# Kernel tuning notes

Hardware: AMD Instinct MI355X
Metric: run time of the kernel (lower is better)

The kernel has to match this reference:

```python
import jax, jax.numpy as jnp
import numpy as np

B, L, H, NH, DH, V, NL = 256, 100, 384, 12, 32, 30000, 6
FF = 4 * H


def _gelu(x):
    c = np.sqrt(2.0 / np.pi).astype(np.float32)
    return x * (0.5 * (1.0 + jnp.tanh(c * (x + 0.044715 * x ** 3))))


def _norm(X, g, b):
    mu = jnp.mean(X, axis=2, keepdims=True)
    var = jnp.var(X, axis=2, ddof=1, keepdims=True)  # torch.var is unbiased
    return g * ((X - mu) / jnp.sqrt(var + 1e-8)) + b


def setup_inputs():
    key = jax.random.key(0)
    ks = jax.random.split(key, 24)
    s = 0.02
    return {
        'x': jax.random.randint(ks[0], (B, L), 0, V, dtype=jnp.int32),
        'seg': jax.random.randint(ks[1], (B, L), 0, 3, dtype=jnp.int32),
        'tok_emb': jax.random.uniform(ks[2], (V, H), jnp.float32, -s, s),
        'seg_emb': jax.random.uniform(ks[3], (3, H), jnp.float32, -s, s),
        'pos_emb': jax.random.normal(ks[4], (L, H), jnp.float32) * 0.05,
        'Wq': jax.random.normal(ks[5], (NL, H, H), jnp.float32) * np.sqrt(2.0 / H).astype(np.float32),
        'bq': jnp.zeros((NL, H), jnp.float32),
        'Wk': jax.random.normal(ks[6], (NL, H, H), jnp.float32) * np.sqrt(2.0 / H).astype(np.float32),
        'bk': jnp.zeros((NL, H), jnp.float32),
        'Wv': jax.random.normal(ks[7], (NL, H, H), jnp.float32) * np.sqrt(2.0 / H).astype(np.float32),
        'bv': jnp.zeros((NL, H), jnp.float32),
        'Wo': jax.random.normal(ks[8], (NL, H, H), jnp.float32) * np.sqrt(2.0 / (2 * H)).astype(np.float32),
        'bo': jnp.zeros((NL, H), jnp.float32),
        'g1': jnp.ones((NL,), jnp.float32),
        'be1': jnp.zeros((NL,), jnp.float32),
        'W1': jax.random.normal(ks[9], (NL, H, FF), jnp.float32) * np.sqrt(2.0 / (H + FF)).astype(np.float32),
        'b1': jnp.zeros((NL, FF), jnp.float32),
        'W2': jax.random.normal(ks[10], (NL, FF, H), jnp.float32) * np.sqrt(2.0 / (H + FF)).astype(np.float32),
        'b2': jnp.zeros((NL, H), jnp.float32),
        'g2': jnp.ones((NL,), jnp.float32),
        'be2': jnp.zeros((NL,), jnp.float32),
        'dropout': 0,
    }


def _encoder_layer(h, pad_mask, nonpad, Wq, bq, Wk, bk, Wv, bv, Wo, bo, g1, be1, W1, b1, W2, b2, g2, be2):
    # --- multi-head self-attention (interleaved head split, as in source) ---
    q = (h @ Wq + bq).reshape(B, L, DH, NH).transpose(3, 0, 1, 2)  # (NH,B,L,DH)
    k = (h @ Wk + bk).reshape(B, L, DH, NH).transpose(3, 0, 3 - 1, 1)  # placeholder
    k = (h @ Wk + bk).reshape(B, L, DH, NH).transpose(3, 0, 2, 1)      # (NH,B,DH,L)
    v = (h @ Wv + bv).reshape(B, L, DH, NH).transpose(3, 0, 1, 2)      # (NH,B,L,DH)
    scale = 1.0 / np.sqrt(H).astype(np.float32)  # d_k = de.shape[-1] = hidden_dim!
    e = jnp.einsum('hbld,hbdm->hblm', q, k) * scale                    # (NH,B,L,L)
    e = jnp.where(pad_mask[None], -1e10, e)
    alpha = jax.nn.softmax(e, axis=-1)
    heads = jnp.einsum('hblm,hbmd->hbld', alpha, v)                    # (NH,B,L,DH)
    a = heads.transpose(1, 2, 0, 3).reshape(B, L, H)  # cat over heads on feature dim
    attn = _norm(a @ Wo + bo + h, g1, be1)
    attn = attn * nonpad
    # --- FFN ---
    f = _gelu(attn @ W1 + b1)
    f = f @ W2 + b2
    out = _norm(f + attn, g2, be2)
    return out * nonpad


def reference(x, seg, tok_emb, seg_emb, pos_emb, Wq, bq, Wk, bk, Wv, bv, Wo, bo,
              g1, be1, W1, b1, W2, b2, g2, be2, dropout):
    pad_mask = (x == 0)[:, None, :] * jnp.ones((1, L, 1), bool)  # (B,L,L)
    nonpad = (x != 0).astype(jnp.float32)[:, :, None]            # (B,L,1), bcast over H
    h = tok_emb[x] + seg_emb[seg] + pos_emb[None, :L]
    h = h * nonpad
    acc = h  # cumulative-sum skip connections: input_i = x_i + ... + x_1
    out = h
    for i in range(NL):
        out = _encoder_layer(acc, pad_mask, nonpad,
                             Wq[i], bq[i], Wk[i], bk[i], Wv[i], bv[i], Wo[i], bo[i],
                             g1[i], be1[i], W1[i], b1[i], W2[i], b2[i], g2[i], be2[i])
        acc = acc + out
    return out
```

## Files before the change

kernel.cpp:

```cpp
#include <hip/hip_runtime.h>
#include <hip/hip_bf16.h>
#include <math.h>

#define B_  256
#define L_  100
#define H_  384
#define NH_ 12
#define DH_ 32
#define NL_ 6
#define FF_ 1536
#define M_  (B_*L_)
#define QKVN 1152

#define LW     3538944
#define OFF_Q  0
#define OFF_K  294912
#define OFF_V  589824
#define OFF_WO 884736
#define OFF_W1 1179648
#define OFF_W2 2359296

typedef __attribute__((ext_vector_type(8))) short short8;
typedef __attribute__((ext_vector_type(4))) float f32x4;

#define GLOBAL_AS __attribute__((address_space(1)))
#define LDS_AS    __attribute__((address_space(3)))

__device__ __forceinline__ void gload_lds16(const void* g, void* l) {
    __builtin_amdgcn_global_load_lds((const GLOBAL_AS void*)g, (LDS_AS void*)l, 16, 0, 0);
}

__device__ __forceinline__ void split2(float v, __hip_bfloat16& hi, __hip_bfloat16& lo) {
    hi = __float2bfloat16(v);
    lo = __float2bfloat16(v - __bfloat162float(hi));
}

__device__ __forceinline__ unsigned short f2b(float v) {
    __hip_bfloat16 h = __float2bfloat16(v);
    return *(unsigned short*)&h;
}

#define VMW(N) asm volatile("s_waitcnt vmcnt(" #N ")" ::: "memory")

__global__ void embed_kernel(const int* __restrict__ x, const int* __restrict__ seg,
                             const float* __restrict__ tok, const float* __restrict__ sege,
                             const float* __restrict__ pos,
                             __hip_bfloat16* __restrict__ acc2) {
    int idx = blockIdx.x * blockDim.x + threadIdx.x;
    if (idx >= M_ * H_) return;
    int m = idx / H_;
    int f = idx - m * H_;
    int t = x[m];
    int s = seg[m];
    int l = m % L_;
    float v = tok[t * H_ + f] + sege[s * H_ + f] + pos[l * H_ + f];
    v = (t != 0) ? v : 0.0f;
    __hip_bfloat16 h, lo;
    split2(v, h, lo);
    acc2[(size_t)m * (2 * H_) + f]      = h;
    acc2[(size_t)m * (2 * H_) + H_ + f] = lo;
}

__global__ void transpose_all_kernel(const float* __restrict__ Wq, const float* __restrict__ Wk,
        const float* __restrict__ Wv, const float* __restrict__ Wo,
        const float* __restrict__ W1, const float* __restrict__ W2,
        __hip_bfloat16* __restrict__ wT) {
    __shared__ float tile[32][33];
    int l = blockIdx.x / 1728;
    int bid = blockIdx.x % 1728;
    const float* src;
    __hip_bfloat16* dst;
    int K, N, nx, tix, perm = 0;
    if (bid < 432) {
        int m = bid / 144; tix = bid % 144;
        src = (m == 0) ? Wq : (m == 1 ? Wk : Wv);
        src += (size_t)l * H_ * H_;
        dst = wT + (size_t)l * LW + (m == 0 ? OFF_Q : (m == 1 ? OFF_K : OFF_V));
        K = 384; N = 384; nx = 12; perm = 1;
    } else if (bid < 576) {
        tix = bid - 432; src = Wo + (size_t)l * H_ * H_;
        dst = wT + (size_t)l * LW + OFF_WO; K = 384; N = 384; nx = 12;
    } else if (bid < 1152) {
        tix = bid - 576; src = W1 + (size_t)l * H_ * FF_;
        dst = wT + (size_t)l * LW + OFF_W1; K = 384; N = 1536; nx = 48;
    } else {
        tix = bid - 1152; src = W2 + (size_t)l * FF_ * H_;
        dst = wT + (size_t)l * LW + OFF_W2; K = 1536; N = 384; nx = 12;
    }
    int n0 = (tix % nx) * 32, k0 = (tix / nx) * 32;
    int tx = threadIdx.x, ty = threadIdx.y;
    #pragma unroll
    for (int i = ty; i < 32; i += 8)
        tile[i][tx] = src[(size_t)(k0 + i) * N + (n0 + tx)];
    __syncthreads();
    #pragma unroll
    for (int i = ty; i < 32; i += 8) {
        float v = tile[tx][i];
        __hip_bfloat16 h, lo;
        split2(v, h, lo);
        int j = n0 + i;
        int jo = perm ? ((j % 12) * 32 + j / 12) : j;
        dst[(size_t)jo * (2 * K) + (k0 + tx)]     = h;
        dst[(size_t)jo * (2 * K) + K + (k0 + tx)] = lo;
    }
}

__global__ void bias_concat_kernel(const float* __restrict__ bq, const float* __restrict__ bk,
                                   const float* __restrict__ bv, float* __restrict__ out) {
    int i = blockIdx.x * 256 + threadIdx.x;
    if (i >= NL_ * QKVN) return;
    int l = i / QKVN, jp = i - l * QKVN;
    int t = jp / 384, r = jp % 384;
    int h = r >> 5, d = r & 31;
    int j = d * 12 + h;
    float v = (t == 0) ? bq[l * 384 + j] : (t == 1 ? bk[l * 384 + j] : bv[l * 384 + j]);
    out[i] = v;
}

template <int TAG, int BIG, int OMODE, int MODEK, int ACT>
__global__ __launch_bounds__(BIG ? 512 : 256) void gemm_bf16_kernel(
        const __hip_bfloat16* __restrict__ A2,
        const __hip_bfloat16* __restrict__ Wt2,
        const float* __restrict__ bias,
        void* __restrict__ outp,
        int N, int K, int nbx) {
    constexpr int BM = BIG ? 256 : 128;
    __shared__ __hip_bfloat16 As[3][BM * 32];
    __shared__ __hip_bfloat16 Bs[3][128 * 32];
    int t = threadIdx.x;
    int lane = t & 63, wv = t >> 6;
    int wm = wv >> 1, wn = wv & 1;

    int nwg = gridDim.x;
    int q8 = nwg >> 3, r8 = nwg & 7;
    int xcd = blockIdx.x & 7, off = blockIdx.x >> 3;
    int swz = (xcd < r8 ? xcd * (q8 + 1) : r8 * (q8 + 1) + (xcd - r8) * q8) + off;
    int bn = (swz % nbx) * 128;
    int bm = (swz / nbx) * BM;

    const int KstA = (MODEK == 2) ? K : 2 * K;
    const int KstW = 2 * K;
    const int Kend = (MODEK == 0) ? 3 * K : 2 * K;
    f32x4 acc[4][4] = {};

    int sr   = t >> 2;
    int sswz = (t & 3) ^ ((t >> 2) & 3) ^ ((t >> 4) & 3);
    const __hip_bfloat16* a_src = A2 + (size_t)(bm + sr) * KstA + sswz * 8;
    const __hip_bfloat16* b_src = Wt2 + (size_t)(bn + sr) * KstW + sswz * 8;

    int slotp = (lane >> 4) ^ (lane & 3) ^ ((lane >> 2) & 3);
    int aOff = (wm * 64 + (lane & 15)) * 32 + slotp * 8;
    int bOff = (wn * 64 + (lane & 15)) * 32 + slotp * 8;

#define STAGE(buf, ak, wk) do { \
        gload_lds16(a_src + (ak), &As[buf][wv * 512]); \
        gload_lds16(a_src + (size_t)(BM / 2) * KstA + (ak), &As[buf][(BM / 2) * 32 + wv * 512]); \
        gload_lds16(b_src + (wk), &Bs[buf][wv * 512]); \
        if (!BIG) gload_lds16(b_src + (size_t)64 * KstW + (wk), &Bs[buf][2048 + wv * 512]); \
    } while (0)

#define KOFFS(k0, ak, wk) do { \
        if (MODEK == 0) { ak = ((k0) < K) ? (k0) : (k0) - K; wk = ((k0) < 2 * K) ? (k0) : (k0) - 2 * K; } \
        else            { ak = ((k0) < K) ? (k0) : (k0) - K; wk = (k0); } \
    } while (0)

    int nt = Kend >> 5;
    {
        int ak, wk;
        KOFFS(0, ak, wk);
        STAGE(0, ak, wk);
        KOFFS(32, ak, wk);
        STAGE(1, ak, wk);
    }
    int c0 = 0, c1 = 1, c2 = 2;
    for (int ti = 0; ti < nt; ++ti) {
        if (ti + 2 < nt) {
            int k2 = (ti + 2) << 5;
            int ak, wk;
            KOFFS(k2, ak, wk);
            STAGE(c2, ak, wk);
            if (BIG) { VMW(6); } else { VMW(8); }
        } else if (ti + 2 == nt) {
            if (BIG) { VMW(3); } else { VMW(4); }
        } else {
            VMW(0);
        }
        __builtin_amdgcn_s_barrier();
        short8 af[4], bf[4];
        #pragma unroll
        for (int m = 0; m < 4; ++m) af[m] = *(const short8*)(&As[c0][aOff + m * 512]);
        #pragma unroll
        for (int n = 0; n < 4; ++n) bf[n] = *(const short8*)(&Bs[c0][bOff + n * 512]);
        __builtin_amdgcn_s_setprio(1);
        #pragma unroll
        for (int m = 0; m < 4; ++m)
            #pragma unroll
            for (int n = 0; n < 4; ++n)
                acc[m][n] = __builtin_amdgcn_mfma_f32_16x16x32_bf16(af[m], bf[n], acc[m][n], 0, 0, 0);
        __builtin_amdgcn_s_setprio(0);
        __builtin_amdgcn_s_barrier();
        int tmp = c0; c0 = c1; c1 = c2; c2 = tmp;
    }
#undef STAGE
#undef KOFFS

    int colBase = bn + wn * 64 + (lane & 15);
    int rowBase = bm + wm * 64 + (lane >> 4) * 4;
    const float c0f = 0.7978845608f;
    #pragma unroll
    for (int n = 0; n < 4; ++n) {
        int c = colBase + n * 16;
        float bvv = bias[c];
        #pragma unroll
        for (int m = 0; m < 4; ++m) {
            int r0 = rowBase + m * 16;
            #pragma unroll
            for (int r = 0; r < 4; ++r) {
                float v = acc[m][n][r] + bvv;
                if (ACT == 1) {
                    float u = c0f * (v + 0.044715f * v * v * v);
                    v = v / (1.0f + __expf(-2.0f * u));
                }
                size_t row = (size_t)(r0 + r);
                if (OMODE == 0) {
                    ((float*)outp)[row * N + c] = v;
                } else {
                    ((__hip_bfloat16*)outp)[row * N + c] = __float2bfloat16(v);
                }
            }
        }
    }
}

__global__ __launch_bounds__(256) void attn_kernel(const __hip_bfloat16* __restrict__ qkvP,
        const int* __restrict__ x, __hip_bfloat16* __restrict__ a2) {
    __shared__ unsigned short qs[112][32];
    __shared__ unsigned short ks[128][32];
    __shared__ unsigned short vst[32][136];
    __shared__ unsigned short ps[112][136];
    __shared__ int xb[128];
    int t = threadIdx.x;
    int lane = t & 63, wv = t >> 6;
    int b = blockIdx.x / NH_;
    int nh = blockIdx.x % NH_;
    const __hip_bfloat16* base = qkvP + (size_t)b * L_ * QKVN;

    for (int i = t; i < 576; i += 256) {
        int d = i / 18, w = i % 18;
        ((int*)vst)[d * 68 + 50 + w] = 0;
    }
    for (int i = t; i < 128; i += 256) xb[i] = (i < L_) ? x[b * L_ + i] : 0;

    {
        int r16 = lane >> 2, s = lane & 3;
        for (int i = wv; i < 7; i += 4) {
            int row = i * 16 + r16;
            int sp = s ^ (row & 3) ^ ((row >> 2) & 3);
            gload_lds16(base + (size_t)row * QKVN + nh * 32 + sp * 8, &qs[i * 16][0]);
        }
        for (int i = wv; i < 8; i += 4) {
            int row = i * 16 + r16;
            int sp = s ^ (row & 3) ^ ((row >> 2) & 3);
            gload_lds16(base + (size_t)row * QKVN + 384 + nh * 32 + sp * 8, &ks[i * 16][0]);
        }
    }
    if (t < 200) {
        int kv = t >> 1, d0 = (t & 1) * 16;
        const __hip_bfloat16* vsrc = base + (size_t)kv * QKVN + 768 + nh * 32 + d0;
        short8 v0 = *(const short8*)vsrc;
        short8 v1 = *(const short8*)(vsrc + 8);
        #pragma unroll
        for (int j = 0; j < 8; ++j) {
            vst[d0 + j][kv]     = (unsigned short)v0[j];
            vst[d0 + 8 + j][kv] = (unsigned short)v1[j];
        }
    }
    __syncthreads();

    const float scale = 1.0f / sqrtf((float)H_);
    int n = lane & 15, g = lane >> 4;

    for (int rt = wv; rt < 7; rt += 4) {
        int arow = rt * 16 + n;
        int asp = (g ^ (arow & 3) ^ ((arow >> 2) & 3)) * 8;
        short8 aq = *(const short8*)&qs[arow][asp];
        f32x4 s8[8];
        #pragma unroll
        for (int ct = 0; ct < 8; ++ct) {
            int brow = ct * 16 + n;
            int bsp = (g ^ (brow & 3) ^ ((brow >> 2) & 3)) * 8;
            short8 bk = *(const short8*)&ks[brow][bsp];
            f32x4 z = {0.0f, 0.0f, 0.0f, 0.0f};
            s8[ct] = __builtin_amdgcn_mfma_f32_16x16x32_bf16(aq, bk, z, 0, 0, 0);
        }
        #pragma unroll
        for (int ct = 0; ct < 8; ++ct) {
            int col = ct * 16 + n;
            int xv = xb[col];
            #pragma unroll
            for (int r = 0; r < 4; ++r) {
                float v = s8[ct][r] * scale;
                v = (xv == 0) ? -1e10f : v;
                v = (col >= L_) ? -INFINITY : v;
                s8[ct][r] = v;
            }
        }
        float sm[4];
        #pragma unroll
        for (int r = 0; r < 4; ++r) {
            float m = s8[0][r];
            #pragma unroll
            for (int ct = 1; ct < 8; ++ct) m = fmaxf(m, s8[ct][r]);
            m = fmaxf(m, __shfl_xor(m, 1, 16));
            m = fmaxf(m, __shfl_xor(m, 2, 16));
            m = fmaxf(m, __shfl_xor(m, 4, 16));
            m = fmaxf(m, __shfl_xor(m, 8, 16));
            float s = 0.0f;
            #pragma unroll
            for (int ct = 0; ct < 8; ++ct) {
                float p = __expf(s8[ct][r] - m);
                s8[ct][r] = p;
                s += p;
            }
            s += __shfl_xor(s, 1, 16);
            s += __shfl_xor(s, 2, 16);
            s += __shfl_xor(s, 4, 16);
            s += __shfl_xor(s, 8, 16);
            sm[r] = s;
        }
        int prow = rt * 16 + g * 4;
        #pragma unroll
        for (int ct = 0; ct < 8; ++ct) {
            int col = ct * 16 + n;
            #pragma unroll
            for (int r = 0; r < 4; ++r)
                ps[prow + r][col] = f2b(s8[ct][r]);
        }
        f32x4 o0 = {0.0f, 0.0f, 0.0f, 0.0f}, o1 = o0;
        #pragma unroll
        for (int kt = 0; kt < 4; ++kt) {
            short8 pa = *(const short8*)&ps[rt * 16 + n][kt * 32 + g * 8];
            short8 b0 = *(const short8*)&vst[n][kt * 32 + g * 8];
            short8 b1 = *(const short8*)&vst[16 + n][kt * 32 + g * 8];
            o0 = __builtin_amdgcn_mfma_f32_16x16x32_bf16(pa, b0, o0, 0, 0, 0);
            o1 = __builtin_amdgcn_mfma_f32_16x16x32_bf16(pa, b1, o1, 0, 0, 0);
        }
        #pragma unroll
        for (int r = 0; r < 4; ++r) {
            int lrow = prow + r;
            if (lrow < L_) {
                size_t row = (size_t)b * L_ + lrow;
                float inv = 1.0f / sm[r];
                __hip_bfloat16 h, lo;
                float v0 = o0[r] * inv;
                split2(v0, h, lo);
                a2[row * (2 * H_) + nh * DH_ + n]      = h;
                a2[row * (2 * H_) + H_ + nh * DH_ + n] = lo;
                float v1 = o1[r] * inv;
                split2(v1, h, lo);
                a2[row * (2 * H_) + nh * DH_ + 16 + n]      = h;
                a2[row * (2 * H_) + H_ + nh * DH_ + 16 + n] = lo;
            }
        }
    }
}

template <int MODE>
__global__ __launch_bounds__(128) void ln_kernel(
        const float* __restrict__ Xf,
        const __hip_bfloat16* __restrict__ R2,
        const int* __restrict__ x,
        const float* __restrict__ gp, const float* __restrict__ bp, int layer,
        float* __restrict__ Yf,
        __hip_bfloat16* __restrict__ Y2,
        __hip_bfloat16* __restrict__ acc2) {
    int row = blockIdx.x;
    int tid = threadIdx.x;
    size_t b1 = (size_t)row * H_;
    size_t b2 = (size_t)row * (2 * H_);

    float v[3];
    #pragma unroll
    for (int j = 0; j < 3; ++j) {
        int f = tid + j * 128;
        float r = __bfloat162float(R2[b2 + f]) + __bfloat162float(R2[b2 + H_ + f]);
        v[j] = Xf[b1 + f] + r;
    }

    __shared__ float red[2];
    float s = v[0] + v[1] + v[2];
    #pragma unroll
    for (int off = 32; off > 0; off >>= 1) s += __shfl_down(s, off);
    if ((tid & 63) == 0) red[tid >> 6] = s;
    __syncthreads();
    float mu = (red[0] + red[1]) * (1.0f / 384.0f);
    __syncthreads();

    float d[3];
    float qq = 0.0f;
    #pragma unroll
    for (int j = 0; j < 3; ++j) { d[j] = v[j] - mu; qq += d[j] * d[j]; }
    #pragma unroll
    for (int off = 32; off > 0; off >>= 1) qq += __shfl_down(qq, off);
    if ((tid & 63) == 0) red[tid >> 6] = qq;
    __syncthreads();
    float var = (red[0] + red[1]) * (1.0f / 383.0f);
    float rstd = rsqrtf(var + 1e-8f);

    float g = gp[layer], bb = bp[layer];
    float np_ = (x[row] != 0) ? 1.0f : 0.0f;
    #pragma unroll
    for (int j = 0; j < 3; ++j) {
        int f = tid + j * 128;
        float y = (g * (d[j] * rstd) + bb) * np_;
        if (MODE == 0) {
            __hip_bfloat16 h, lo;
            split2(y, h, lo);
            Y2[b2 + f]      = h;
            Y2[b2 + H_ + f] = lo;
        } else {
            Yf[b1 + f] = y;
            float a = __bfloat162float(acc2[b2 + f]) + __bfloat162float(acc2[b2 + H_ + f]) + y;
            __hip_bfloat16 h, lo;
            split2(a, h, lo);
            acc2[b2 + f]      = h;
            acc2[b2 + H_ + f] = lo;
        }
    }
}

extern "C" void kernel_launch(void* const* d_in, const int* in_sizes, int n_in,
                              void* d_out, int out_size, void* d_ws, size_t ws_size,
                              hipStream_t stream) {
    const int*   x    = (const int*)d_in[0];
    const int*   seg  = (const int*)d_in[1];
    const float* tok  = (const float*)d_in[2];
    const float* sege = (const float*)d_in[3];
    const float* pos  = (const float*)d_in[4];
    const float* Wq   = (const float*)d_in[5];
    const float* bq   = (const float*)d_in[6];
    const float* Wk   = (const float*)d_in[7];
    const float* bk   = (const float*)d_in[8];
    const float* Wv   = (const float*)d_in[9];
    const float* bv   = (const float*)d_in[10];
    const float* Wo   = (const float*)d_in[11];
    const float* bo   = (const float*)d_in[12];
    const float* g1   = (const float*)d_in[13];
    const float* be1  = (const float*)d_in[14];
    const float* W1   = (const float*)d_in[15];
    const float* b1   = (const float*)d_in[16];
    const float* W2   = (const float*)d_in[17];
    const float* b2   = (const float*)d_in[18];
    const float* g2   = (const float*)d_in[19];
    const float* be2  = (const float*)d_in[20];

    char* p = (char*)d_ws;
    __hip_bfloat16* wT   = (__hip_bfloat16*)p; p += (size_t)NL_ * LW * 2;
    __hip_bfloat16* acc2 = (__hip_bfloat16*)p; p += 39321600;
    __hip_bfloat16* bE2  = (__hip_bfloat16*)p; p += 39321600;
    float* qkvb          = (float*)p;          p += 27648;
    char* pool           = p;
    __hip_bfloat16* qkvP = (__hip_bfloat16*)pool;
    __hip_bfloat16* bA2  = (__hip_bfloat16*)(pool + 58982400);
    float*          woF  = (float*)pool;
    __hip_bfloat16* f2   = (__hip_bfloat16*)pool;
    float* out = (float*)d_out;

    transpose_all_kernel<<<dim3(1728 * NL_), dim3(32, 8), 0, stream>>>(Wq, Wk, Wv, Wo, W1, W2, wT);
    bias_concat_kernel<<<dim3((NL_ * QKVN + 255) / 256), dim3(256), 0, stream>>>(bq, bk, bv, qkvb);
    embed_kernel<<<dim3((M_ * H_ + 255) / 256), dim3(256), 0, stream>>>(x, seg, tok, sege, pos, acc2);

    for (int l = 0; l < NL_; ++l) {
        const __hip_bfloat16* wTL = wT + (size_t)l * LW;
        const float* bol = bo + (size_t)l * H_;
        const float* b1l = b1 + (size_t)l * FF_;
        const float* b2l = b2 + (size_t)l * H_;

        gemm_bf16_kernel<0, 1, 2, 0, 0><<<dim3((QKVN / 128) * (M_ / 256)), dim3(512), 0, stream>>>(
            acc2, wTL + OFF_Q, qkvb + (size_t)l * QKVN, qkvP, QKVN, H_, QKVN / 128);
        attn_kernel<<<dim3(B_ * NH_), dim3(256), 0, stream>>>(qkvP, x, bA2);
        gemm_bf16_kernel<1, 0, 0, 0, 0><<<dim3((H_ / 128) * (M_ / 128)), dim3(256), 0, stream>>>(
            bA2, wTL + OFF_WO, bol, woF, H_, H_, H_ / 128);
        ln_kernel<0><<<dim3(M_), dim3(128), 0, stream>>>(
            woF, acc2, x, g1, be1, l, nullptr, bE2, nullptr);
        gemm_bf16_kernel<2, 1, 2, 0, 1><<<dim3((FF_ / 128) * (M_ / 256)), dim3(512), 0, stream>>>(
            bE2, wTL + OFF_W1, b1l, f2, FF_, H_, FF_ / 128);
        gemm_bf16_kernel<3, 0, 0, 2, 0><<<dim3((H_ / 128) * (M_ / 128)), dim3(256), 0, stream>>>(
            f2, wTL + OFF_W2, b2l, out, H_, FF_, H_ / 128);
        ln_kernel<1><<<dim3(M_), dim3(128), 0, stream>>>(
            out, bE2, x, g2, be2, l, out, nullptr, acc2);
    }
}
```

Baseline: 2.532 ms.

## Add 256x256-tile quad-buffered GEMM for FFN up-projection with fused GELU

```diff
diff --git a/kernel.cpp b/kernel.cpp
--- a/kernel.cpp
+++ b/kernel.cpp
@@ -232,6 +232,115 @@
     }
 }
 
+__global__ __launch_bounds__(512) void gemm_8q_kernel(
+        const __hip_bfloat16* __restrict__ A2,
+        const __hip_bfloat16* __restrict__ Wt2,
+        const float* __restrict__ bias,
+        __hip_bfloat16* __restrict__ outp,
+        int N, int K, int nbx) {
+    __shared__ __hip_bfloat16 As[4][256 * 32];
+    __shared__ __hip_bfloat16 Bs[4][256 * 32];
+    int t = threadIdx.x;
+    int lane = t & 63, wv = t >> 6;
+    int wm = wv >> 2, wn = wv & 3;
+
+    int nwg = gridDim.x;
+    int q8 = nwg >> 3, r8 = nwg & 7;
+    int xcd = blockIdx.x & 7, off = blockIdx.x >> 3;
+    int swz = (xcd < r8 ? xcd * (q8 + 1) : r8 * (q8 + 1) + (xcd - r8) * q8) + off;
+    int bn = (swz % nbx) * 256;
+    int bm = (swz / nbx) * 256;
+
+    const int Kst  = 2 * K;
+    const int Kend = 3 * K;
+    f32x4 acc[8][4] = {};
+
+    int sr   = t >> 2;
+    int sswz = (t & 3) ^ ((t >> 2) & 3) ^ ((t >> 4) & 3);
+    const __hip_bfloat16* a_src = A2 + (size_t)(bm + sr) * Kst + sswz * 8;
+    const __hip_bfloat16* b_src = Wt2 + (size_t)(bn + sr) * Kst + sswz * 8;
+
+    int slotp = (lane >> 4) ^ (lane & 3) ^ ((lane >> 2) & 3);
+    int lm = lane & 15;
+    int aBase = (wm * 128 + lm) * 32 + slotp * 8;
+    int bBase = (wn * 64 + lm) * 32 + slotp * 8;
+
+#define STAGE8(buf, ak, wk) do { \
+        gload_lds16(a_src + (ak), &As[buf][wv * 512]); \
+        gload_lds16(a_src + (size_t)128 * Kst + (ak), &As[buf][4096 + wv * 512]); \
+        gload_lds16(b_src + (wk), &Bs[buf][wv * 512]); \
+        gload_lds16(b_src + (size_t)128 * Kst + (wk), &Bs[buf][4096 + wv * 512]); \
+    } while (0)
+#define KOFFS8(k0, ak, wk) do { \
+        ak = ((k0) < K) ? (k0) : (k0) - K; \
+        wk = ((k0) < 2 * K) ? (k0) : (k0) - 2 * K; \
+    } while (0)
+
+    int nt = Kend >> 5;
+    {
+        int ak, wk;
+        KOFFS8(0, ak, wk);  STAGE8(0, ak, wk);
+        KOFFS8(32, ak, wk); STAGE8(1, ak, wk);
+        KOFFS8(64, ak, wk); STAGE8(2, ak, wk);
+    }
+    for (int kt = 0; kt < nt; ++kt) {
+        int cur = kt & 3;
+        if (kt + 3 < nt) {
+            int k3 = (kt + 3) << 5;
+            int ak, wk;
+            KOFFS8(k3, ak, wk);
+            STAGE8((kt + 3) & 3, ak, wk);
+            VMW(12);
+        } else if (kt + 3 == nt) {
+            VMW(8);
+        } else if (kt + 2 == nt) {
+            VMW(4);
+        } else {
+            VMW(0);
+        }
+        __builtin_amdgcn_s_barrier();
+        short8 bf[4];
+        #pragma unroll
+        for (int nf = 0; nf < 4; ++nf)
+            bf[nf] = *(const short8*)(&Bs[cur][bBase + nf * 512]);
+        #pragma unroll
+        for (int q = 0; q < 4; ++q) {
+            short8 af0 = *(const short8*)(&As[cur][aBase + (2 * q) * 512]);
+            short8 af1 = *(const short8*)(&As[cur][aBase + (2 * q + 1) * 512]);
+            __builtin_amdgcn_s_setprio(1);
+            #pragma unroll
+            for (int nf = 0; nf < 4; ++nf) {
+                acc[2 * q][nf]     = __builtin_amdgcn_mfma_f32_16x16x32_bf16(af0, bf[nf], acc[2 * q][nf], 0, 0, 0);
+                acc[2 * q + 1][nf] = __builtin_amdgcn_mfma_f32_16x16x32_bf16(af1, bf[nf], acc[2 * q + 1][nf], 0, 0, 0);
+            }
+            __builtin_amdgcn_s_setprio(0);
+            __builtin_amdgcn_s_barrier();
+        }
+    }
+#undef STAGE8
+#undef KOFFS8
+
+    int colBase = bn + wn * 64 + lm;
+    int rowBase = bm + wm * 128 + (lane >> 4) * 4;
+    const float c0f = 0.7978845608f;
+    #pragma unroll
+    for (int nf = 0; nf < 4; ++nf) {
+        int c = colBase + nf * 16;
+        float bvv = bias[c];
+        #pragma unroll
+        for (int mf = 0; mf < 8; ++mf) {
+            int r0 = rowBase + mf * 16;
+            #pragma unroll
+            for (int r = 0; r < 4; ++r) {
+                float v = acc[mf][nf][r] + bvv;
+                float u = c0f * (v + 0.044715f * v * v * v);
+                v = v / (1.0f + __expf(-2.0f * u));
+                outp[(size_t)(r0 + r) * N + c] = __float2bfloat16(v);
+            }
+        }
+    }
+}
+
 __global__ __launch_bounds__(256) void attn_kernel(const __hip_bfloat16* __restrict__ qkvP,
         const int* __restrict__ x, __hip_bfloat16* __restrict__ a2) {
     __shared__ unsigned short qs[112][32];
@@ -483,8 +592,8 @@
             bA2, wTL + OFF_WO, bol, woF, H_, H_, H_ / 128);
         ln_kernel<0><<<dim3(M_), dim3(128), 0, stream>>>(
             woF, acc2, x, g1, be1, l, nullptr, bE2, nullptr);
-        gemm_bf16_kernel<2, 1, 2, 0, 1><<<dim3((FF_ / 128) * (M_ / 256)), dim3(512), 0, stream>>>(
-            bE2, wTL + OFF_W1, b1l, f2, FF_, H_, FF_ / 128);
+        gemm_8q_kernel<<<dim3((FF_ / 256) * (M_ / 256)), dim3(512), 0, stream>>>(
+            bE2, wTL + OFF_W1, b1l, f2, FF_, H_, FF_ / 256);
         gemm_bf16_kernel<3, 0, 0, 2, 0><<<dim3((H_ / 128) * (M_ / 128)), dim3(256), 0, stream>>>(
             f2, wTL + OFF_W2, b2l, out, H_, FF_, H_ / 128);
         ln_kernel<1><<<dim3(M_), dim3(128), 0, stream>>>(
```

New measurement: 2.831 ms. +11.8%, slower.
